# Kernel tuning notes

Hardware: AMD Instinct MI355X
Metric: run time of the kernel (lower is better)

Reference implementation:

```python
import jax, jax.numpy as jnp
import numpy as np

NUM_FREQUENCIES = 128
NUM_TIMES = 128
SIGMA = 0.1
BATCH = 32
LENGTH = 8192


def setup_inputs() -> dict:
    key = jax.random.key(0)
    signal = jax.random.normal(key, (BATCH, LENGTH), dtype=jnp.float32)
    return {"signal": signal}


def reference(signal) -> jnp.ndarray:
    # signal: [B, L]
    B, L = signal.shape
    # Matches torch.linspace(...).long(): linspace then truncate toward zero.
    time_centers = jnp.linspace(0.0, L - 1, NUM_TIMES).astype(jnp.int32).astype(jnp.float32)  # [T]
    freq_vals = jnp.linspace(0.0, L // 2, NUM_FREQUENCIES).astype(jnp.int32).astype(jnp.float32)  # [F]
    t = jnp.arange(L, dtype=jnp.float32)  # [L]
    sigma_w = SIGMA * L
    # Gaussian windows, one per time center: [T, L]
    window = jnp.exp(-0.5 * ((t[None, :] - time_centers[:, None]) / sigma_w) ** 2)
    # Real part of exp(-2j*pi*f*l/L) modulation: [F, L]
    two_pi = jnp.float32(2.0 * np.pi)
    cos_mod = jnp.cos(two_pi * freq_vals[:, None] * t[None, :] / L)
    # Original loop stores a complex dot product into a real tensor -> real part only:
    # result[b, f, t] = sum_l signal[b,l] * window[t,l] * cos(2*pi*f*l/L)
    windowed = jnp.einsum('bl,tl->btl', signal, window)  # [B, T, L]
    result = jnp.einsum('btl,fl->bft', windowed, cos_mod)  # [B, F, T]
    return result
```

## Files before the change

kernel.cpp:

```cpp
#include <hip/hip_runtime.h>
#include <hip/hip_bf16.h>
#include <math.h>


#define L_ 8192
#define B_ 32

typedef _Float16 half8 __attribute__((ext_vector_type(8)));
typedef __fp16 fp16x2 __attribute__((ext_vector_type(2)));
typedef float float2v __attribute__((ext_vector_type(2)));
typedef float float4v __attribute__((ext_vector_type(4)));

#define H_ 0.001220703125f
#define CSTEP_ 7.66990393942594528198e-4f

__global__ __launch_bounds__(512, 2) void gabor_kernel(
    const float* __restrict__ signal, float* __restrict__ out) {
  const int bx = blockIdx.x;
  const int bp = bx & 15;
  const int th = (bx >> 4) & 3;
  const int fh = (bx >> 6) & 3;
  const int tid = threadIdx.x;
  const int lane = tid & 63;
  const int wv = tid >> 6;
  const int frow = lane & 15;
  const int quad = lane >> 4;

  __shared__ __align__(16) char smraw[32768];
  _Float16(*Sg)[L_] = (_Float16(*)[L_])smraw;
  float4v(*Acc)[64][4] = (float4v(*)[64][4])smraw;

  {
#pragma unroll
    for (int bi = 0; bi < 2; ++bi) {
      const float* srow = signal + (size_t)(2 * bp + bi) * L_;
#pragma unroll
      for (int i = 0; i < 2; ++i) {
        const int off = i * 4096 + tid * 8;
        float4v s0 = *(const float4v*)(srow + off);
        float4v s1 = *(const float4v*)(srow + off + 4);
        union { fp16x2 h2[4]; half8 h8; } sh;
        sh.h2[0] = __builtin_amdgcn_cvt_pkrtz(s0[0], s0[1]);
        sh.h2[1] = __builtin_amdgcn_cvt_pkrtz(s0[2], s0[3]);
        sh.h2[2] = __builtin_amdgcn_cvt_pkrtz(s1[0], s1[1]);
        sh.h2[3] = __builtin_amdgcn_cvt_pkrtz(s1[2], s1[3]);
        *(half8*)&Sg[bi][off] = sh.h8;
      }
    }
  }
  __syncthreads();

  const int t0 = th * 32;
  const int f0 = fh * 32;
  const int k0 = wv * 1024 + quad * 8;

  float2v w2[2][4], Rw2[2][4];
  float2v cE2[2][4], cO2[2][4];
  float2v K32v[2];
  const float2v Q32v = {0.99847528338432312012f,
                        0.99847528338432312012f};
#pragma unroll
  for (int fr = 0; fr < 2; ++fr) {
    const float tc = truncf((float)(t0 + fr * 16 + frow) * (8191.0f / 127.0f));
    const int fv = (int)((float)(f0 + fr * 16 + frow) * (4096.0f / 127.0f));
    const float K32 = 2.0f * __cosf((float)((fv * 32) & (L_ - 1)) * CSTEP_);
    K32v[fr] = (float2v){K32, K32};
#pragma unroll
    for (int q = 0; q < 4; ++q) {
#pragma unroll
      for (int h = 0; h < 2; ++h) {
        const int j = 2 * q + h;
        const float x = ((float)(k0 + j) - tc) * H_;
        w2[fr][q][h] = __expf(-0.5f * x * x);
        Rw2[fr][q][h] =
            __expf(__builtin_fmaf(-0.0390625f, x, -7.62939453125e-4f));
        cE2[fr][q][h] = __cosf((float)((fv * (k0 + j)) & (L_ - 1)) * CSTEP_);
        cO2[fr][q][h] =
            __cosf((float)((fv * (k0 + j + 8160)) & (L_ - 1)) * CSTEP_);
      }
    }
  }

  float4v acc[2][2][2];
#pragma unroll
  for (int i = 0; i < 2; ++i)
#pragma unroll
    for (int j = 0; j < 2; ++j)
#pragma unroll
      for (int bi = 0; bi < 2; ++bi) acc[i][j][bi] = (float4v)(0.0f);

  union H8 { fp16x2 h2[4]; half8 h8; };

#pragma unroll 1
  for (int p = 0; p < 16; ++p) {
    {
      H8 ha[2], hc[2];
#pragma unroll
      for (int fr = 0; fr < 2; ++fr)
#pragma unroll
        for (int q = 0; q < 4; ++q) {
          ha[fr].h2[q] = __builtin_amdgcn_cvt_pkrtz(w2[fr][q][0], w2[fr][q][1]);
          hc[fr].h2[q] = __builtin_amdgcn_cvt_pkrtz(cE2[fr][q][0], cE2[fr][q][1]);
        }
      const int kk = k0 + (2 * p) * 32;
      const half8 sg0 = *(const half8*)&Sg[0][kk];
      const half8 sg1 = *(const half8*)&Sg[1][kk];
#pragma unroll
      for (int fr2 = 0; fr2 < 2; ++fr2) {
        const half8 hb0 = hc[fr2].h8 * sg0;
        const half8 hb1 = hc[fr2].h8 * sg1;
        acc[0][fr2][0] = __builtin_amdgcn_mfma_f32_16x16x32_f16(
            ha[0].h8, hb0, acc[0][fr2][0], 0, 0, 0);
        acc[1][fr2][0] = __builtin_amdgcn_mfma_f32_16x16x32_f16(
            ha[1].h8, hb0, acc[1][fr2][0], 0, 0, 0);
        acc[0][fr2][1] = __builtin_amdgcn_mfma_f32_16x16x32_f16(
            ha[0].h8, hb1, acc[0][fr2][1], 0, 0, 0);
        acc[1][fr2][1] = __builtin_amdgcn_mfma_f32_16x16x32_f16(
            ha[1].h8, hb1, acc[1][fr2][1], 0, 0, 0);
      }
#pragma unroll
      for (int fr = 0; fr < 2; ++fr)
#pragma unroll
        for (int q = 0; q < 4; ++q) {
          w2[fr][q] *= Rw2[fr][q];
          Rw2[fr][q] *= Q32v;
          cO2[fr][q] = __builtin_elementwise_fma(K32v[fr], cE2[fr][q], -cO2[fr][q]);
        }
    }
    {
      H8 ha[2], hc[2];
#pragma unroll
      for (int fr = 0; fr < 2; ++fr)
#pragma unroll
        for (int q = 0; q < 4; ++q) {
          ha[fr].h2[q] = __builtin_amdgcn_cvt_pkrtz(w2[fr][q][0], w2[fr][q][1]);
          hc[fr].h2[q] = __builtin_amdgcn_cvt_pkrtz(cO2[fr][q][0], cO2[fr][q][1]);
        }
      const int kk = k0 + (2 * p + 1) * 32;
      const half8 sg0 = *(const half8*)&Sg[0][kk];
      const half8 sg1 = *(const half8*)&Sg[1][kk];
#pragma unroll
      for (int fr2 = 0; fr2 < 2; ++fr2) {
        const half8 hb0 = hc[fr2].h8 * sg0;
        const half8 hb1 = hc[fr2].h8 * sg1;
        acc[0][fr2][0] = __builtin_amdgcn_mfma_f32_16x16x32_f16(
            ha[0].h8, hb0, acc[0][fr2][0], 0, 0, 0);
        acc[1][fr2][0] = __builtin_amdgcn_mfma_f32_16x16x32_f16(
            ha[1].h8, hb0, acc[1][fr2][0], 0, 0, 0);
        acc[0][fr2][1] = __builtin_amdgcn_mfma_f32_16x16x32_f16(
            ha[0].h8, hb1, acc[0][fr2][1], 0, 0, 0);
        acc[1][fr2][1] = __builtin_amdgcn_mfma_f32_16x16x32_f16(
            ha[1].h8, hb1, acc[1][fr2][1], 0, 0, 0);
      }
#pragma unroll
      for (int fr = 0; fr < 2; ++fr)
#pragma unroll
        for (int q = 0; q < 4; ++q) {
          w2[fr][q] *= Rw2[fr][q];
          Rw2[fr][q] *= Q32v;
          cE2[fr][q] = __builtin_elementwise_fma(K32v[fr], cO2[fr][q], -cE2[fr][q]);
        }
    }
  }

#pragma unroll
  for (int bi = 0; bi < 2; ++bi) {
    __syncthreads();
#pragma unroll
    for (int i4 = 0; i4 < 4; ++i4)
      Acc[wv][lane][i4] = acc[i4 >> 1][i4 & 1][bi];
    __syncthreads();
    if (wv < 4) {
      float4v sum = Acc[0][lane][wv];
#pragma unroll
      for (int w = 1; w < 8; ++w) sum += Acc[w][lane][wv];
      const int fr1 = wv >> 1, fr2 = wv & 1;
      const int f = f0 + fr2 * 16 + frow;
      const int t = t0 + fr1 * 16 + quad * 4;
      *(float4v*)(out + ((size_t)((2 * bp + bi) * 128 + f)) * 128 + t) = sum;
    }
  }
}

extern "C" void kernel_launch(void* const* d_in, const int* in_sizes, int n_in,
                              void* d_out, int out_size, void* d_ws, size_t ws_size,
                              hipStream_t stream) {
  const float* signal = (const float*)d_in[0];
  float* out = (float*)d_out;
  gabor_kernel<<<dim3(256), dim3(512), 0, stream>>>(signal, out);
}
```

Baseline: 68.03 us.

## Switch to 32x32x16 MFMA tiles to cut per-lane window/cosine recurrence work

Replaces the 2x2 grid of 16x16x32 MFMAs with a single 32x32x16 MFMA per batch row. Each lane now covers one of 32 rows, so the Gaussian-window and cosine recurrences track one row instead of two. That halves the VALU work for generating operands and for packed fp16 conversion. The K step per MFMA halves to 16, so the recurrence constants and loop count change, and the accumulator layout and output indexing are remapped to match.

```diff
diff --git a/kernel.cpp b/kernel.cpp
--- a/kernel.cpp
+++ b/kernel.cpp
@@ -10,9 +10,13 @@
 typedef __fp16 fp16x2 __attribute__((ext_vector_type(2)));
 typedef float float2v __attribute__((ext_vector_type(2)));
 typedef float float4v __attribute__((ext_vector_type(4)));
+typedef float float16v __attribute__((ext_vector_type(16)));
 
 #define H_ 0.001220703125f
 #define CSTEP_ 7.66990393942594528198e-4f
+#define DLT_ 0.01953125f
+#define DLT2H_ 1.9073486328125e-4f
+#define Q16_ 0.99961860303f
 
 __global__ __launch_bounds__(512, 2) void gabor_kernel(
     const float* __restrict__ signal, float* __restrict__ out) {
@@ -23,143 +27,107 @@
   const int tid = threadIdx.x;
   const int lane = tid & 63;
   const int wv = tid >> 6;
-  const int frow = lane & 15;
-  const int quad = lane >> 4;
+  const int row32 = lane & 31;
+  const int kg = lane >> 5;
 
   __shared__ __align__(16) char smraw[32768];
   _Float16(*Sg)[L_] = (_Float16(*)[L_])smraw;
   float4v(*Acc)[64][4] = (float4v(*)[64][4])smraw;
 
-  {
 #pragma unroll
-    for (int bi = 0; bi < 2; ++bi) {
-      const float* srow = signal + (size_t)(2 * bp + bi) * L_;
+  for (int bi = 0; bi < 2; ++bi) {
+    const float* srow = signal + (size_t)(2 * bp + bi) * L_;
 #pragma unroll
-      for (int i = 0; i < 2; ++i) {
-        const int off = i * 4096 + tid * 8;
-        float4v s0 = *(const float4v*)(srow + off);
-        float4v s1 = *(const float4v*)(srow + off + 4);
-        union { fp16x2 h2[4]; half8 h8; } sh;
-        sh.h2[0] = __builtin_amdgcn_cvt_pkrtz(s0[0], s0[1]);
-        sh.h2[1] = __builtin_amdgcn_cvt_pkrtz(s0[2], s0[3]);
-        sh.h2[2] = __builtin_amdgcn_cvt_pkrtz(s1[0], s1[1]);
-        sh.h2[3] = __builtin_amdgcn_cvt_pkrtz(s1[2], s1[3]);
-        *(half8*)&Sg[bi][off] = sh.h8;
-      }
+    for (int i = 0; i < 2; ++i) {
+      const int off = i * 4096 + tid * 8;
+      float4v s0 = *(const float4v*)(srow + off);
+      float4v s1 = *(const float4v*)(srow + off + 4);
+      union { fp16x2 h2[4]; half8 h8; } sh;
+      sh.h2[0] = __builtin_amdgcn_cvt_pkrtz(s0[0], s0[1]);
+      sh.h2[1] = __builtin_amdgcn_cvt_pkrtz(s0[2], s0[3]);
+      sh.h2[2] = __builtin_amdgcn_cvt_pkrtz(s1[0], s1[1]);
+      sh.h2[3] = __builtin_amdgcn_cvt_pkrtz(s1[2], s1[3]);
+      *(half8*)&Sg[bi][off] = sh.h8;
     }
   }
   __syncthreads();
 
   const int t0 = th * 32;
   const int f0 = fh * 32;
-  const int k0 = wv * 1024 + quad * 8;
+  const int k0 = wv * 1024 + kg * 8;
 
-  float2v w2[2][4], Rw2[2][4];
-  float2v cE2[2][4], cO2[2][4];
-  float2v K32v[2];
-  const float2v Q32v = {0.99847528338432312012f,
-                        0.99847528338432312012f};
-#pragma unroll
-  for (int fr = 0; fr < 2; ++fr) {
-    const float tc = truncf((float)(t0 + fr * 16 + frow) * (8191.0f / 127.0f));
-    const int fv = (int)((float)(f0 + fr * 16 + frow) * (4096.0f / 127.0f));
-    const float K32 = 2.0f * __cosf((float)((fv * 32) & (L_ - 1)) * CSTEP_);
-    K32v[fr] = (float2v){K32, K32};
+  float2v w2[4], Rw2[4];
+  float2v cE2[4], cO2[4];
+  float2v K16v;
+  const float2v Q16v = {Q16_, Q16_};
+  {
+    const float tc = truncf((float)(t0 + row32) * (8191.0f / 127.0f));
+    const int fv = (int)((float)(f0 + row32) * (4096.0f / 127.0f));
+    const float K16 = 2.0f * __cosf((float)((fv * 16) & (L_ - 1)) * CSTEP_);
+    K16v = (float2v){K16, K16};
 #pragma unroll
     for (int q = 0; q < 4; ++q) {
 #pragma unroll
       for (int h = 0; h < 2; ++h) {
         const int j = 2 * q + h;
         const float x = ((float)(k0 + j) - tc) * H_;
-        w2[fr][q][h] = __expf(-0.5f * x * x);
-        Rw2[fr][q][h] =
-            __expf(__builtin_fmaf(-0.0390625f, x, -7.62939453125e-4f));
-        cE2[fr][q][h] = __cosf((float)((fv * (k0 + j)) & (L_ - 1)) * CSTEP_);
-        cO2[fr][q][h] =
-            __cosf((float)((fv * (k0 + j + 8160)) & (L_ - 1)) * CSTEP_);
+        w2[q][h] = __expf(-0.5f * x * x);
+        Rw2[q][h] = __expf(__builtin_fmaf(-DLT_, x, -DLT2H_));
+        cE2[q][h] = __cosf((float)((fv * (k0 + j)) & (L_ - 1)) * CSTEP_);
+        cO2[q][h] =
+            __cosf((float)((fv * (k0 + j + 8176)) & (L_ - 1)) * CSTEP_);
       }
     }
   }
 
-  float4v acc[2][2][2];
-#pragma unroll
-  for (int i = 0; i < 2; ++i)
-#pragma unroll
-    for (int j = 0; j < 2; ++j)
-#pragma unroll
-      for (int bi = 0; bi < 2; ++bi) acc[i][j][bi] = (float4v)(0.0f);
+  float16v acc[2];
+  acc[0] = (float16v)(0.0f);
+  acc[1] = (float16v)(0.0f);
 
   union H8 { fp16x2 h2[4]; half8 h8; };
 
 #pragma unroll 1
-  for (int p = 0; p < 16; ++p) {
+  for (int p = 0; p < 32; ++p) {
+    const int kbase = k0 + p * 32;
     {
-      H8 ha[2], hc[2];
+      H8 ha, hc;
 #pragma unroll
-      for (int fr = 0; fr < 2; ++fr)
-#pragma unroll
-        for (int q = 0; q < 4; ++q) {
-          ha[fr].h2[q] = __builtin_amdgcn_cvt_pkrtz(w2[fr][q][0], w2[fr][q][1]);
-          hc[fr].h2[q] = __builtin_amdgcn_cvt_pkrtz(cE2[fr][q][0], cE2[fr][q][1]);
-        }
-      const int kk = k0 + (2 * p) * 32;
-      const half8 sg0 = *(const half8*)&Sg[0][kk];
-      const half8 sg1 = *(const half8*)&Sg[1][kk];
-#pragma unroll
-      for (int fr2 = 0; fr2 < 2; ++fr2) {
-        const half8 hb0 = hc[fr2].h8 * sg0;
-        const half8 hb1 = hc[fr2].h8 * sg1;
-        acc[0][fr2][0] = __builtin_amdgcn_mfma_f32_16x16x32_f16(
-            ha[0].h8, hb0, acc[0][fr2][0], 0, 0, 0);
-        acc[1][fr2][0] = __builtin_amdgcn_mfma_f32_16x16x32_f16(
-            ha[1].h8, hb0, acc[1][fr2][0], 0, 0, 0);
-        acc[0][fr2][1] = __builtin_amdgcn_mfma_f32_16x16x32_f16(
-            ha[0].h8, hb1, acc[0][fr2][1], 0, 0, 0);
-        acc[1][fr2][1] = __builtin_amdgcn_mfma_f32_16x16x32_f16(
-            ha[1].h8, hb1, acc[1][fr2][1], 0, 0, 0);
+      for (int q = 0; q < 4; ++q) {
+        ha.h2[q] = __builtin_amdgcn_cvt_pkrtz(w2[q][0], w2[q][1]);
+        hc.h2[q] = __builtin_amdgcn_cvt_pkrtz(cE2[q][0], cE2[q][1]);
       }
 #pragma unroll
-      for (int fr = 0; fr < 2; ++fr)
-#pragma unroll
-        for (int q = 0; q < 4; ++q) {
-          w2[fr][q] *= Rw2[fr][q];
-          Rw2[fr][q] *= Q32v;
-          cO2[fr][q] = __builtin_elementwise_fma(K32v[fr], cE2[fr][q], -cO2[fr][q]);
-        }
+      for (int q = 0; q < 4; ++q) {
+        w2[q] *= Rw2[q];
+        Rw2[q] *= Q16v;
+        cO2[q] = __builtin_elementwise_fma(K16v, cE2[q], -cO2[q]);
+      }
+      const half8 sg0 = *(const half8*)&Sg[0][kbase];
+      const half8 sg1 = *(const half8*)&Sg[1][kbase];
+      acc[0] = __builtin_amdgcn_mfma_f32_32x32x16_f16(ha.h8, hc.h8 * sg0,
+                                                      acc[0], 0, 0, 0);
+      acc[1] = __builtin_amdgcn_mfma_f32_32x32x16_f16(ha.h8, hc.h8 * sg1,
+                                                      acc[1], 0, 0, 0);
     }
     {
-      H8 ha[2], hc[2];
+      H8 ha, hc;
 #pragma unroll
-      for (int fr = 0; fr < 2; ++fr)
-#pragma unroll
-        for (int q = 0; q < 4; ++q) {
-          ha[fr].h2[q] = __builtin_amdgcn_cvt_pkrtz(w2[fr][q][0], w2[fr][q][1]);
-          hc[fr].h2[q] = __builtin_amdgcn_cvt_pkrtz(cO2[fr][q][0], cO2[fr][q][1]);
-        }
-      const int kk = k0 + (2 * p + 1) * 32;
-      const half8 sg0 = *(const half8*)&Sg[0][kk];
-      const half8 sg1 = *(const half8*)&Sg[1][kk];
-#pragma unroll
-      for (int fr2 = 0; fr2 < 2; ++fr2) {
-        const half8 hb0 = hc[fr2].h8 * sg0;
-        const half8 hb1 = hc[fr2].h8 * sg1;
-        acc[0][fr2][0] = __builtin_amdgcn_mfma_f32_16x16x32_f16(
-            ha[0].h8, hb0, acc[0][fr2][0], 0, 0, 0);
-        acc[1][fr2][0] = __builtin_amdgcn_mfma_f32_16x16x32_f16(
-            ha[1].h8, hb0, acc[1][fr2][0], 0, 0, 0);
-        acc[0][fr2][1] = __builtin_amdgcn_mfma_f32_16x16x32_f16(
-            ha[0].h8, hb1, acc[0][fr2][1], 0, 0, 0);
-        acc[1][fr2][1] = __builtin_amdgcn_mfma_f32_16x16x32_f16(
-            ha[1].h8, hb1, acc[1][fr2][1], 0, 0, 0);
+      for (int q = 0; q < 4; ++q) {
+        ha.h2[q] = __builtin_amdgcn_cvt_pkrtz(w2[q][0], w2[q][1]);
+        hc.h2[q] = __builtin_amdgcn_cvt_pkrtz(cO2[q][0], cO2[q][1]);
       }
 #pragma unroll
-      for (int fr = 0; fr < 2; ++fr)
-#pragma unroll
-        for (int q = 0; q < 4; ++q) {
-          w2[fr][q] *= Rw2[fr][q];
-          Rw2[fr][q] *= Q32v;
-          cE2[fr][q] = __builtin_elementwise_fma(K32v[fr], cO2[fr][q], -cE2[fr][q]);
-        }
+      for (int q = 0; q < 4; ++q) {
+        w2[q] *= Rw2[q];
+        Rw2[q] *= Q16v;
+        cE2[q] = __builtin_elementwise_fma(K16v, cO2[q], -cE2[q]);
+      }
+      const half8 sg0 = *(const half8*)&Sg[0][kbase + 16];
+      const half8 sg1 = *(const half8*)&Sg[1][kbase + 16];
+      acc[0] = __builtin_amdgcn_mfma_f32_32x32x16_f16(ha.h8, hc.h8 * sg0,
+                                                      acc[0], 0, 0, 0);
+      acc[1] = __builtin_amdgcn_mfma_f32_32x32x16_f16(ha.h8, hc.h8 * sg1,
+                                                      acc[1], 0, 0, 0);
     }
   }
 
@@ -167,16 +135,18 @@
   for (int bi = 0; bi < 2; ++bi) {
     __syncthreads();
 #pragma unroll
-    for (int i4 = 0; i4 < 4; ++i4)
-      Acc[wv][lane][i4] = acc[i4 >> 1][i4 & 1][bi];
+    for (int g = 0; g < 4; ++g) {
+      float4v v = {acc[bi][4 * g], acc[bi][4 * g + 1], acc[bi][4 * g + 2],
+                   acc[bi][4 * g + 3]};
+      Acc[wv][lane][g] = v;
+    }
     __syncthreads();
     if (wv < 4) {
       float4v sum = Acc[0][lane][wv];
 #pragma unroll
       for (int w = 1; w < 8; ++w) sum += Acc[w][lane][wv];
-      const int fr1 = wv >> 1, fr2 = wv & 1;
-      const int f = f0 + fr2 * 16 + frow;
-      const int t = t0 + fr1 * 16 + quad * 4;
+      const int f = f0 + (lane & 31);
+      const int t = t0 + 8 * wv + 4 * (lane >> 5);
       *(float4v*)(out + ((size_t)((2 * bp + bi) * 128 + f)) * 128 + t) = sum;
     }
   }
```

Result: no change. 67.80 us (-0.3%).
